# Optimization experiments

Hardware: AMD Instinct MI355X
Metric: run time of the kernel (lower is better)

The kernel has to match this reference:

```python
import jax, jax.numpy as jnp
import numpy as np
import math

Z_DIM = 512
RADIUS = 64
K_TERMS = 700  # power-series length; ample for v=255, kappa<=800


def log_ive(v, x):
    """log(ive(v, x)) = log(I_v(x) * exp(-x)) via log-space power series.

    I_v(x) = sum_k (x/2)^(v+2k) / (k! * Gamma(v+k+1)); summed stably with
    logsumexp. x: [B,1] -> returns [B,1].
    """
    ks = jnp.arange(K_TERMS, dtype=x.dtype)
    # k-dependent log-gamma factors, shape [K]
    lg = jax.lax.lgamma(ks + 1.0) + jax.lax.lgamma(ks + v + 1.0)
    log_half_x = jnp.log(0.5 * x)                      # [B,1]
    terms = 2.0 * ks * log_half_x[..., None] - lg      # [B,1,K]
    return v * log_half_x + jax.nn.logsumexp(terms, axis=-1) - x


def setup_inputs() -> dict:
    key = jax.random.key(0)
    k1, k2, k3 = jax.random.split(key, 3)
    B, d = 65536, Z_DIM
    mu = jax.random.normal(k1, (B, d), dtype=jnp.float32)
    mu = mu / jnp.linalg.norm(mu, axis=1, keepdims=True)
    wc = jax.random.normal(k2, (B, d), dtype=jnp.float32)
    wc = wc / jnp.linalg.norm(wc, axis=1, keepdims=True) * RADIUS
    # realistic vMF concentrations
    kappa = jax.random.uniform(k3, (B, 1), dtype=jnp.float32) * 600.0 + 200.0
    return {"mu": mu, "kappa": kappa, "wc": wc}


def reference(mu, kappa, wc):
    d = float(Z_DIM)
    r = float(RADIUS)
    v = d / 2.0 - 1.0
    log_ive_kappa = jnp.log(1e-6 + jnp.exp(log_ive(v, kappa)))  # [B,1]
    log_iv_kappa = log_ive_kappa + kappa
    cos_theta = jnp.sum(mu * wc, axis=1, keepdims=True) / r      # [B,1]
    l1 = -kappa * cos_theta
    l2 = -(d / 2.0 - 1.0) * jnp.log(1e-6 + kappa)
    l3 = log_iv_kappa * 1.0
    losses = l1 + l2 + l3 + d / 2.0 * math.log(2.0 * math.pi) + d * math.log(r)
    return (losses, l1, l2, l3)
```

## Files before the change

kernel.cpp:

```cpp
#include <hip/hip_runtime.h>
#include <math.h>


#define K_TERMS 700
#define WND 256
#define ZD 512
#define VV 255.0f
#define CONST_TERM 2599.8446676805443f

__global__ __launch_bounds__(256) void lg_table_kernel(float* __restrict__ lg) {
    __shared__ double ssum[256];
    const int t = threadIdx.x;
    double loc[3];
    double tot = 0.0;
    #pragma unroll
    for (int i = 0; i < 3; ++i) {
        int p = t * 3 + i;
        double inc = 0.0;
        if (p >= 1 && p < K_TERMS)
            inc = log((double)p) + log((double)(p + 255));
        tot += inc;
        loc[i] = tot;
    }
    ssum[t] = tot;
    __syncthreads();
    for (int off = 1; off < 256; off <<= 1) {
        double v = (t >= off) ? ssum[t - off] : 0.0;
        __syncthreads();
        ssum[t] += v;
        __syncthreads();
    }
    const double excl = (t == 0) ? 0.0 : ssum[t - 1];
    const double z = 256.0;
    const double base = (z - 0.5) * log(z) - z + 0.918938533204672741780
                      + 1.0 / (12.0 * z) - 1.0 / (360.0 * z * z * z);
    #pragma unroll
    for (int i = 0; i < 3; ++i) {
        int p = t * 3 + i;
        if (p < K_TERMS) lg[p] = (float)(base + excl + loc[i]);
    }
}

__global__ __launch_bounds__(256) void vmf_kernel(
    const float* __restrict__ mu, const float* __restrict__ kappa,
    const float* __restrict__ wc, const float* __restrict__ lg,
    float* __restrict__ out, int B)
{
    const int wave = (int)((blockIdx.x * blockDim.x + threadIdx.x) >> 6);
    const int lane = (int)(threadIdx.x & 63);
    if (wave >= B) return;

    const float4* m4 = (const float4*)(mu + (size_t)wave * ZD) + lane * 2;
    const float4* w4 = (const float4*)(wc + (size_t)wave * ZD) + lane * 2;
    float4 a0 = m4[0], a1 = m4[1];
    float4 b0 = w4[0], b1 = w4[1];

    const float kap = kappa[wave];
    const float L   = logf(0.5f * kap);

    const float kstar = 0.5f * (sqrtf(65025.0f + kap * kap) - 255.0f);
    int klo = (int)kstar - (WND / 2);
    klo = klo < 0 ? 0 : (klo > (K_TERMS - WND) ? (K_TERMS - WND) : klo);

    float t0, t1, t2, t3;
    {
        const int k0 = klo + lane;
        t0 = fmaf(2.0f * (float)(k0),        L, -lg[k0]);
        t1 = fmaf(2.0f * (float)(k0 + 64),   L, -lg[k0 + 64]);
        t2 = fmaf(2.0f * (float)(k0 + 128),  L, -lg[k0 + 128]);
        t3 = fmaf(2.0f * (float)(k0 + 192),  L, -lg[k0 + 192]);
    }
    float m = fmaxf(fmaxf(t0, t1), fmaxf(t2, t3));
    #pragma unroll
    for (int off = 32; off >= 1; off >>= 1)
        m = fmaxf(m, __shfl_xor(m, off, 64));
    float s = __expf(t0 - m) + __expf(t1 - m) + __expf(t2 - m) + __expf(t3 - m);
    #pragma unroll
    for (int off = 32; off >= 1; off >>= 1)
        s += __shfl_xor(s, off, 64);
    const float lse = m + logf(s);

    float dp = a0.x * b0.x + a0.y * b0.y + a0.z * b0.z + a0.w * b0.w
             + a1.x * b1.x + a1.y * b1.y + a1.z * b1.z + a1.w * b1.w;
    #pragma unroll
    for (int off = 32; off >= 1; off >>= 1)
        dp += __shfl_xor(dp, off, 64);

    const float log_ive      = VV * L + lse - kap;
    const float log_ive_kap  = logf(1e-6f + __expf(log_ive));
    const float log_iv_kappa = log_ive_kap + kap;
    const float cos_theta    = dp * (1.0f / 64.0f);

    const float l1 = -kap * cos_theta;
    const float l2 = -VV * logf(1e-6f + kap);
    const float l3 = log_iv_kappa;
    const float losses = l1 + l2 + l3 + CONST_TERM;

    if (lane == 0) {
        out[wave]                 = losses;
        out[(size_t)B + wave]     = l1;
        out[(size_t)2 * B + wave] = l2;
        out[(size_t)3 * B + wave] = l3;
    }
}

extern "C" void kernel_launch(void* const* d_in, const int* in_sizes, int n_in,
                              void* d_out, int out_size, void* d_ws, size_t ws_size,
                              hipStream_t stream) {
    const float* mu    = (const float*)d_in[0];
    const float* kappa = (const float*)d_in[1];
    const float* wc    = (const float*)d_in[2];
    float* out = (float*)d_out;
    float* lg  = (float*)d_ws;
    const int B = in_sizes[1];

    lg_table_kernel<<<1, 256, 0, stream>>>(lg);
    vmf_kernel<<<(B + 3) / 4, 256, 0, stream>>>(mu, kappa, wc, lg, out, B);
}
```

Baseline: 276.9 us.

## Process four rows per wave with 16-lane groups and halve logsumexp window

Each wave now splits into four 16-lane groups, and each group handles one row. Every lane loads 8 float4 pairs for the dot product and evaluates 8 series terms. The log-sum-exp window drops from 256 to 128 terms around the peak term, and the shuffle reductions shrink to 4 steps. This cuts the launch to a quarter as many blocks and raises per-lane memory-level parallelism, aiming to lower reduction and transcendental overhead. The narrower window may lose accuracy for terms outside it.

```diff
diff --git a/kernel.cpp b/kernel.cpp
--- a/kernel.cpp
+++ b/kernel.cpp
@@ -3,7 +3,7 @@
 
 
 #define K_TERMS 700
-#define WND 256
+#define WND 128
 #define ZD 512
 #define VV 255.0f
 #define CONST_TERM 2599.8446676805443f
@@ -46,45 +46,56 @@
     const float* __restrict__ wc, const float* __restrict__ lg,
     float* __restrict__ out, int B)
 {
-    const int wave = (int)((blockIdx.x * blockDim.x + threadIdx.x) >> 6);
-    const int lane = (int)(threadIdx.x & 63);
-    if (wave >= B) return;
+    const int tid  = (int)threadIdx.x;
+    const int wv   = tid >> 6;
+    const int lane = tid & 63;
+    const int grp  = lane >> 4;
+    const int sub  = lane & 15;
+    const int row  = ((int)blockIdx.x * 4 + wv) * 4 + grp;
+    if (row >= B) return;
 
-    const float4* m4 = (const float4*)(mu + (size_t)wave * ZD) + lane * 2;
-    const float4* w4 = (const float4*)(wc + (size_t)wave * ZD) + lane * 2;
-    float4 a0 = m4[0], a1 = m4[1];
-    float4 b0 = w4[0], b1 = w4[1];
+    const float kap = kappa[row];
 
-    const float kap = kappa[wave];
-    const float L   = logf(0.5f * kap);
+    const float4* m4 = (const float4*)(mu + (size_t)row * ZD);
+    const float4* w4 = (const float4*)(wc + (size_t)row * ZD);
+    float dp = 0.0f;
+    #pragma unroll
+    for (int j = 0; j < 8; ++j) {
+        float4 a = m4[sub + 16 * j];
+        float4 b = w4[sub + 16 * j];
+        dp += a.x * b.x + a.y * b.y + a.z * b.z + a.w * b.w;
+    }
+
+    const float L = logf(0.5f * kap);
 
     const float kstar = 0.5f * (sqrtf(65025.0f + kap * kap) - 255.0f);
     int klo = (int)kstar - (WND / 2);
     klo = klo < 0 ? 0 : (klo > (K_TERMS - WND) ? (K_TERMS - WND) : klo);
 
-    float t0, t1, t2, t3;
-    {
-        const int k0 = klo + lane;
-        t0 = fmaf(2.0f * (float)(k0),        L, -lg[k0]);
-        t1 = fmaf(2.0f * (float)(k0 + 64),   L, -lg[k0 + 64]);
-        t2 = fmaf(2.0f * (float)(k0 + 128),  L, -lg[k0 + 128]);
-        t3 = fmaf(2.0f * (float)(k0 + 192),  L, -lg[k0 + 192]);
+    float t[8];
+    #pragma unroll
+    for (int j = 0; j < 8; ++j) {
+        int k = klo + sub + 16 * j;
+        t[j] = fmaf((float)(2 * k), L, -lg[k]);
     }
-    float m = fmaxf(fmaxf(t0, t1), fmaxf(t2, t3));
+    float m = t[0];
     #pragma unroll
-    for (int off = 32; off >= 1; off >>= 1)
+    for (int j = 1; j < 8; ++j) m = fmaxf(m, t[j]);
+    #pragma unroll
+    for (int off = 8; off >= 1; off >>= 1)
         m = fmaxf(m, __shfl_xor(m, off, 64));
-    float s = __expf(t0 - m) + __expf(t1 - m) + __expf(t2 - m) + __expf(t3 - m);
+    float s = 0.0f;
     #pragma unroll
-    for (int off = 32; off >= 1; off >>= 1)
+    for (int j = 0; j < 8; ++j) s += __expf(t[j] - m);
+    #pragma unroll
+    for (int off = 8; off >= 1; off >>= 1)
         s += __shfl_xor(s, off, 64);
+
+    #pragma unroll
+    for (int off = 8; off >= 1; off >>= 1)
+        dp += __shfl_xor(dp, off, 64);
+
     const float lse = m + logf(s);
-
-    float dp = a0.x * b0.x + a0.y * b0.y + a0.z * b0.z + a0.w * b0.w
-             + a1.x * b1.x + a1.y * b1.y + a1.z * b1.z + a1.w * b1.w;
-    #pragma unroll
-    for (int off = 32; off >= 1; off >>= 1)
-        dp += __shfl_xor(dp, off, 64);
 
     const float log_ive      = VV * L + lse - kap;
     const float log_ive_kap  = logf(1e-6f + __expf(log_ive));
@@ -96,11 +107,11 @@
     const float l3 = log_iv_kappa;
     const float losses = l1 + l2 + l3 + CONST_TERM;
 
-    if (lane == 0) {
-        out[wave]                 = losses;
-        out[(size_t)B + wave]     = l1;
-        out[(size_t)2 * B + wave] = l2;
-        out[(size_t)3 * B + wave] = l3;
+    if (sub == 0) {
+        out[row]                 = losses;
+        out[(size_t)B + row]     = l1;
+        out[(size_t)2 * B + row] = l2;
+        out[(size_t)3 * B + row] = l3;
     }
 }
 
@@ -115,5 +126,5 @@
     const int B = in_sizes[1];
 
     lg_table_kernel<<<1, 256, 0, stream>>>(lg);
-    vmf_kernel<<<(B + 3) / 4, 256, 0, stream>>>(mu, kappa, wc, lg, out, B);
+    vmf_kernel<<<(B + 15) / 16, 256, 0, stream>>>(mu, kappa, wc, lg, out, B);
 }
```

New measurement: 277.3 us. Within noise of the previous version (+0.2%).
